# Performance work log

Measured on AMD Instinct MI355X. Metric: run time of the kernel, lower is better.

## Reference

```python
import jax, jax.numpy as jnp
import numpy as np
import math

B, T, D, CAP = 4, 1024, 512, 32768
MEM_UPDATE_MOMENTUM = 0.99
MEM_NEW_DATA_RATE = 0.01

def setup_inputs() -> dict:
    key = jax.random.key(0)
    k1, k2, k3, k4, k5 = jax.random.split(key, 5)
    keys = jax.random.normal(k1, (B, T, D), dtype=jnp.float32)
    values = jax.random.normal(k2, (B, T, D), dtype=jnp.float32)
    importance = jax.random.uniform(k3, (B, T, 1), dtype=jnp.float32)
    query = jax.random.normal(k4, (B, T, D), dtype=jnp.float32)
    # xavier_uniform on (1, CAP, D): fan_in=D, fan_out=CAP (torch treats dim-1/dim-2)
    bound = math.sqrt(6.0 / (CAP + D))
    mem = jax.random.uniform(k5, (1, CAP, D), minval=-bound, maxval=bound, dtype=jnp.float32)
    return {"keys": keys, "values": values, "importance": importance, "query": query, "mem": mem}

def reference(keys, values, importance, query, mem):
    b, t, d = keys.shape
    cap = mem.shape[1]
    # ---- write ----
    scores = jnp.einsum('btd,ocd->btc', keys, mem)          # [b, t, cap]
    usage = jax.nn.softmax(scores, axis=-1).sum(axis=1)     # [b, cap]
    combined = importance.mean(axis=(1, 2))                 # [b]
    write_priority = combined[:, None] + 0.1 * usage        # [b, cap]
    k = min(t, cap)
    _, indices = jax.lax.top_k(write_priority, k)           # [b, k]
    values_write = values[:, :k]                            # [b, k, d]
    scatter = jnp.zeros((b, cap, d), dtype=keys.dtype)
    scatter = scatter.at[jnp.arange(b)[:, None], indices].set(values_write)
    new_mem = mem * MEM_UPDATE_MOMENTUM + scatter.mean(axis=0, keepdims=True) * MEM_NEW_DATA_RATE
    # ---- read (against updated memory) ----
    attn = jnp.einsum('bqd,ocd->bqc', query, new_mem) / math.sqrt(d)
    attn = jax.nn.softmax(attn, axis=-1)                    # [b, q, cap]
    out = jnp.einsum('bqc,ocd->bqd', attn, new_mem)         # [b, q, d]
    return out
```

## Files before the change

kernel.cpp:

```cpp
#include <hip/hip_runtime.h>
#include <hip/hip_fp8.h>

typedef float f32x4 __attribute__((ext_vector_type(4)));
typedef float f32x16 __attribute__((ext_vector_type(16)));
typedef short s16x8 __attribute__((ext_vector_type(8)));
typedef short s16x4 __attribute__((ext_vector_type(4)));
typedef unsigned short ush;
typedef unsigned char u8;

constexpr int Bn = 4, Tn = 1024, Dn = 512, CAPn = 32768, Kn = 1024;
constexpr int ROWS = Bn * Tn;
constexpr float SCALE = 0.044194173824159216f;
constexpr float SC64 = SCALE / 64.0f;
constexpr float MOM = 0.99f;
constexpr float RATE_B = 0.0025f;

constexpr size_t OFF_NM8   = 0;
constexpr size_t OFF_NMT   = 33554432;
constexpr size_t OFF_OPART = 67108864;
constexpr size_t OFF_KHF   = 67108864;
constexpr size_t OFF_ZPART = 75497472;
constexpr size_t OFF_PRIO  = 83886080;
constexpr size_t OFF_RANK  = 84410368;
constexpr size_t OFF_COMB  = 84934656;
constexpr size_t OFF_ZP2   = 100663296;

#define MFMA(a, b, c) __builtin_amdgcn_mfma_f32_16x16x32_bf16((a), (b), (c), 0, 0, 0)
#define MFMAH(a, b, c) __builtin_amdgcn_mfma_f32_16x16x32_f16((a), (b), (c), 0, 0, 0)
#define MFMA8(a, b, c) __builtin_amdgcn_mfma_f32_16x16x32_fp8_fp8((a), (b), (c), 0, 0, 0)
#define MFMAB32(a, b, c) __builtin_amdgcn_mfma_f32_32x32x16_bf16((a), (b), (c), 0, 0, 0)

__device__ __forceinline__ ush bfrn(float x) {
  unsigned u = __float_as_uint(x);
  return (ush)((u + 0x7FFFu + ((u >> 16) & 1u)) >> 16);
}
__device__ __forceinline__ float bff(ush h) { return __uint_as_float(((unsigned)h) << 16); }
__device__ __forceinline__ ush f16rn(float x) {
  _Float16 h = (_Float16)x;
  return *(ush*)&h;
}
__device__ __forceinline__ u8 f8rn(float x) {
  __hip_fp8_e4m3 v(x);
  return (u8)v.__x;
}

__device__ __forceinline__ void gl16(const void* g, void* l) {
  __builtin_amdgcn_global_load_lds(
      (const __attribute__((address_space(1))) void*)(uintptr_t)g,
      (__attribute__((address_space(3))) void*)(uintptr_t)l, 16, 0, 0);
}

__global__ void k_combined(const float* __restrict__ imp, float* __restrict__ comb) {
  __shared__ float red[256];
  int b = blockIdx.x;
  float s = 0.f;
  for (int t = threadIdx.x; t < Tn; t += 256) s += imp[(size_t)b * Tn + t];
  red[threadIdx.x] = s;
  __syncthreads();
  for (int off = 128; off > 0; off >>= 1) {
    if (threadIdx.x < (unsigned)off) red[threadIdx.x] += red[threadIdx.x + off];
    __syncthreads();
  }
  if (threadIdx.x == 0) comb[b] = red[0] * (1.0f / Tn);
}

__global__ void k_cvt_f16(const float* __restrict__ x, ush* __restrict__ o) {
  size_t i = ((size_t)blockIdx.x * 256 + threadIdx.x) * 4;
  f32x4 v = *(const f32x4*)&x[i];
  s16x4 h;
#pragma unroll
  for (int j = 0; j < 4; ++j) h[j] = (short)f16rn(v[j]);
  *(s16x4*)&o[i] = h;
}

__global__ __launch_bounds__(256, 2) void k_rowexp(const ush* __restrict__ Ahf,
                                                   const ush* __restrict__ Bhf,
                                                   float* __restrict__ zpart) {
  __shared__ ush Bs[64 * 512];
  __shared__ float red[2][64];
  const int tid = threadIdx.x;
  const int lane = tid & 63, wid = tid >> 6;
  const int wc2 = wid >> 1, wt = wid & 1;
  const int l15 = lane & 15, g = lane >> 4;
  const int cb = blockIdx.x;
  const int cBase = cb * 64;

  s16x8 afr[2][16];
#pragma unroll
  for (int mi = 0; mi < 2; ++mi) {
    int c = cBase + wc2 * 32 + mi * 16 + l15;
#pragma unroll
    for (int ks = 0; ks < 16; ++ks)
      afr[mi][ks] = *(const s16x8*)&Ahf[(size_t)c * Dn + ks * 32 + g * 8];
  }

  for (int tt = 0; tt < 64; ++tt) {
    const int tBase = tt * 64;
#pragma unroll
    for (int rr = 0; rr < 16; ++rr) {
      int idx = rr * 256 + tid;
      int row = idx >> 6, ch = idx & 63;
      gl16(&Bhf[(size_t)(tBase + row) * Dn + ((ch ^ (row & 7)) << 3)],
           &Bs[rr * 2048 + wid * 512]);
    }
    __syncthreads();
    f32x4 S[2][2];
#pragma unroll
    for (int mi = 0; mi < 2; ++mi)
#pragma unroll
      for (int ni = 0; ni < 2; ++ni) S[mi][ni] = (f32x4){0.f, 0.f, 0.f, 0.f};
#pragma unroll
    for (int ks = 0; ks < 16; ++ks) {
      s16x8 bfr[2];
#pragma unroll
      for (int ni = 0; ni < 2; ++ni) {
        int trow = wt * 32 + ni * 16 + l15;
        bfr[ni] = *(const s16x8*)&Bs[trow * 512 + (((ks * 4 + g) ^ (trow & 7)) * 8)];
      }
#pragma unroll
      for (int mi = 0; mi < 2; ++mi)
#pragma unroll
        for (int ni = 0; ni < 2; ++ni) S[mi][ni] = MFMAH(afr[mi][ks], bfr[ni], S[mi][ni]);
    }
    float tacc[2] = {0.f, 0.f};
#pragma unroll
    for (int mi = 0; mi < 2; ++mi)
#pragma unroll
      for (int ni = 0; ni < 2; ++ni)
#pragma unroll
        for (int r = 0; r < 4; ++r) tacc[ni] += __expf(S[mi][ni][r]);
#pragma unroll
    for (int ni = 0; ni < 2; ++ni) {
      float v = tacc[ni];
      v += __shfl_xor(v, 16);
      v += __shfl_xor(v, 32);
      tacc[ni] = v;
    }
    if (g == 0) {
      red[wc2][wt * 32 + l15] = tacc[0];
      red[wc2][wt * 32 + 16 + l15] = tacc[1];
    }
    __syncthreads();
    if (tid < 64) zpart[(size_t)cb * ROWS + tBase + tid] = red[0][tid] + red[1][tid];
  }
}

__global__ void k_invl(const float* __restrict__ zpart, float* __restrict__ invl) {
  int t = blockIdx.x * 256 + threadIdx.x;
  float s = 0.f;
  for (int cb = 0; cb < 512; ++cb) s += zpart[(size_t)cb * ROWS + t];
  invl[t] = 1.0f / s;
}

__global__ __launch_bounds__(256, 3) void k_usage(const ush* __restrict__ mhf,
                                                  const ush* __restrict__ khf,
                                                  const float* __restrict__ invl,
                                                  const float* __restrict__ comb,
                                                  float* __restrict__ prio) {
  __shared__ ush Ah[128 * 64], Bh[128 * 64];
  const int tid = threadIdx.x;
  const int lane = tid & 63, w = tid >> 6;
  const int l15 = lane & 15, g = lane >> 4;
  const int cBase = blockIdx.x * 128;
  const int b = blockIdx.y;
  const ush* khb = khf + (size_t)b * Tn * Dn;
  const int r0 = tid >> 3, u0 = tid & 7;
  const int usw = (u0 ^ (r0 & 7)) << 3;

  float uacc[2][4] = {{0.f, 0.f, 0.f, 0.f}, {0.f, 0.f, 0.f, 0.f}};
  for (int tt = 0; tt < 8; ++tt) {
    f32x4 S[2][8];
#pragma unroll
    for (int mi = 0; mi < 2; ++mi)
#pragma unroll
      for (int ni = 0; ni < 8; ++ni) S[mi][ni] = (f32x4){0.f, 0.f, 0.f, 0.f};
    for (int kk = 0; kk < 8; ++kk) {
      __syncthreads();
      {
        size_t a0 = (size_t)(cBase + r0) * Dn + kk * 64 + usw;
        size_t a1 = (size_t)(cBase + r0 + 64) * Dn + kk * 64 + usw;
        gl16(&mhf[a0], &Ah[w * 512]);
        gl16(&mhf[a1], &Ah[4096 + w * 512]);
        size_t b0 = (size_t)(tt * 128 + r0) * Dn + kk * 64 + usw;
        size_t b1 = (size_t)(tt * 128 + r0 + 64) * Dn + kk * 64 + usw;
        gl16(&khb[b0], &Bh[w * 512]);
        gl16(&khb[b1], &Bh[4096 + w * 512]);
      }
      __syncthreads();
#pragma unroll
      for (int ks2 = 0; ks2 < 2; ++ks2) {
        s16x8 ah[2];
#pragma unroll
        for (int mi = 0; mi < 2; ++mi) {
          int crow = w * 32 + mi * 16 + l15;
          ah[mi] = *(const s16x8*)&Ah[crow * 64 + (((ks2 * 4 + g) ^ (crow & 7)) * 8)];
        }
#pragma unroll
        for (int ni = 0; ni < 8; ++ni) {
          int trow = ni * 16 + l15;
          s16x8 bh = *(const s16x8*)&Bh[trow * 64 + (((ks2 * 4 + g) ^ (trow & 7)) * 8)];
#pragma unroll
          for (int mi = 0; mi < 2; ++mi) S[mi][ni] = MFMAH(ah[mi], bh, S[mi][ni]);
        }
      }
    }
#pragma unroll
    for (int ni = 0; ni < 8; ++ni) {
      float il = invl[b * Tn + tt * 128 + ni * 16 + l15];
#pragma unroll
      for (int mi = 0; mi < 2; ++mi)
#pragma unroll
        for (int r = 0; r < 4; ++r) uacc[mi][r] += __expf(S[mi][ni][r]) * il;
    }
  }
#pragma unroll
  for (int mi = 0; mi < 2; ++mi)
#pragma unroll
    for (int r = 0; r < 4; ++r) {
      float v = uacc[mi][r];
      v += __shfl_xor(v, 1);
      v += __shfl_xor(v, 2);
      v += __shfl_xor(v, 4);
      v += __shfl_xor(v, 8);
      if (l15 == 0)
        prio[(size_t)b * CAPn + cBase + w * 32 + mi * 16 + g * 4 + r] =
            comb[b] + 0.1f * v;
    }
}

__global__ void k_rankinit(int* __restrict__ rank) {
  rank[blockIdx.x * 256 + threadIdx.x] = Kn;
}

__global__ __launch_bounds__(1024) void k_select(const float* __restrict__ prio,
                                                 int* __restrict__ rank) {
  const int b = blockIdx.x;
  const float* p = prio + (size_t)b * CAPn;
  __shared__ int hist[256];
  __shared__ unsigned long long s_pref;
  __shared__ int s_krem;
  __shared__ int s_cnt;
  __shared__ unsigned long long selk[Kn];
  const int tid = threadIdx.x;
  if (tid == 0) { s_pref = 0ull; s_krem = Kn; s_cnt = 0; }

#define KEYOF(c, kk)                                                         \
  {                                                                          \
    unsigned mb_ = __float_as_uint(p[(c)]);                                  \
    mb_ = (mb_ & 0x80000000u) ? ~mb_ : (mb_ | 0x80000000u);                  \
    (kk) = ((unsigned long long)mb_ << 32) | (unsigned)(0xFFFFFFFFu - (c));  \
  }

  __syncthreads();
  for (int pos = 56; pos >= 0; pos -= 8) {
    if (tid < 256) hist[tid] = 0;
    __syncthreads();
    unsigned long long pref = s_pref;
    unsigned long long maskhi = (pos == 56) ? 0ull : (~0ull << (pos + 8));
    for (int c = tid; c < CAPn; c += 1024) {
      unsigned long long k;
      KEYOF(c, k);
      if ((k & maskhi) == pref) atomicAdd(&hist[(int)((k >> pos) & 255)], 1);
    }
    __syncthreads();
    if (tid == 0) {
      int krem = s_krem;
      int d = 255;
      for (;; --d) {
        int h = hist[d];
        if (krem <= h || d == 0) break;
        krem -= h;
      }
      s_pref = pref | ((unsigned long long)d << pos);
      s_krem = krem;
    }
    __syncthreads();
  }
  unsigned long long T = s_pref;
  for (int c = tid; c < CAPn; c += 1024) {
    unsigned long long k;
    KEYOF(c, k);
    if (k >= T) {
      int idx = atomicAdd(&s_cnt, 1);
      selk[idx] = k;
    }
  }
  __syncthreads();
  unsigned long long mine = selk[tid];
  int r = 0;
  for (int j = 0; j < Kn; ++j) r += (selk[j] > mine) ? 1 : 0;
  int c = (int)(0xFFFFFFFFu - (unsigned)(mine & 0xFFFFFFFFull));
  rank[(size_t)b * CAPn + c] = r;
#undef KEYOF
}

__global__ void k_newmem8(const float* __restrict__ mem, const float* __restrict__ values,
                          const int* __restrict__ rank, u8* __restrict__ nm8) {
  int gid = blockIdx.x * 256 + threadIdx.x;
  int c = gid >> 7;
  int q = (gid & 127) << 2;
  f32x4 m = *(const f32x4*)&mem[(size_t)c * Dn + q];
  f32x4 acc = {0.f, 0.f, 0.f, 0.f};
#pragma unroll
  for (int b = 0; b < Bn; ++b) {
    int r = rank[(size_t)b * CAPn + c];
    if (r < Kn) acc += *(const f32x4*)&values[((size_t)b * Tn + r) * Dn + q];
  }
  f32x4 res = (m * MOM + acc * RATE_B) * 64.0f;
  union { u8 b[4]; unsigned w; } out;
#pragma unroll
  for (int j = 0; j < 4; ++j) out.b[j] = f8rn(res[j]);
  *(unsigned*)&nm8[(size_t)c * Dn + q] = out.w;
}

__global__ __launch_bounds__(256) void k_nmT(const float* __restrict__ mem,
                                             const float* __restrict__ values,
                                             const int* __restrict__ rank,
                                             ush* __restrict__ nmT) {
  __shared__ ush tile[64][65];
  int cBase = blockIdx.x * 64, dBase = blockIdx.y * 64;
  int tid = threadIdx.x;
  int c = tid >> 2, dq = (tid & 3) * 16;
  int rr[4];
#pragma unroll
  for (int b = 0; b < Bn; ++b) rr[b] = rank[(size_t)b * CAPn + cBase + c];
#pragma unroll
  for (int j = 0; j < 4; ++j) {
    f32x4 m = *(const f32x4*)&mem[(size_t)(cBase + c) * Dn + dBase + dq + j * 4];
    f32x4 a = {0.f, 0.f, 0.f, 0.f};
#pragma unroll
    for (int b = 0; b < Bn; ++b)
      if (rr[b] < Kn)
        a += *(const f32x4*)&values[((size_t)b * Tn + rr[b]) * Dn + dBase + dq + j * 4];
    f32x4 res = m * MOM + a * RATE_B;
#pragma unroll
    for (int jj = 0; jj < 4; ++jj) tile[c][dq + j * 4 + jj] = bfrn(res[jj]);
  }
  __syncthreads();
  int drow = tid >> 2, cq = (tid & 3) * 16;
#pragma unroll
  for (int k = 0; k < 2; ++k) {
    s16x8 v;
#pragma unroll
    for (int j = 0; j < 8; ++j) v[j] = (short)tile[cq + k * 8 + j][drow];
    *(s16x8*)&nmT[(size_t)(dBase + drow) * CAPn + cBase + cq + k * 8] = v;
  }
}

#define WAITV2 asm volatile("s_waitcnt vmcnt(2)" ::: "memory")
#define WAITL0 asm volatile("s_waitcnt lgkmcnt(0)" ::: "memory")
#define BAR __builtin_amdgcn_s_barrier()
__global__ __launch_bounds__(512, 1) void k_attnout(
    const float* __restrict__ query, const u8* __restrict__ nm8,
    const ush* __restrict__ nmT, ush* __restrict__ opart,
    float* __restrict__ zp2) {
  __shared__ __align__(16) u8 L[131072];
  __shared__ float zred[128];
  __shared__ float zacc[128];
  constexpr int LMS = 0, LMT = 49152, LPS = 98304;
  const int tid = threadIdx.x;
  const int lane = tid & 63, w = tid >> 6;
  const int l15 = lane & 15, g = lane >> 4;
  const int l31 = lane & 31, h = lane >> 5;
  const int dt = w & 3, qg = w >> 2;
  const int cy = blockIdx.x;
  const int qBase = blockIdx.y * 128;
  const int q = w * 16 + l15;
  const int r0 = tid >> 3, u0 = tid & 7;
  const int usw = (u0 ^ (r0 & 7)) << 3;
  const int usw8 = (u0 ^ (r0 & 7)) << 4;

  auto stage_ms = [&](int buf, int cb_, int kk) {
    const u8* src = nm8 + (size_t)cb_ * Dn + kk * 128;
    gl16(&src[(size_t)r0 * Dn + usw8], &L[LMS + buf * 16384 + w * 1024]);
    gl16(&src[(size_t)(r0 + 64) * Dn + usw8], &L[LMS + buf * 16384 + 8192 + w * 1024]);
  };
  auto stage_mt = [&](int buf, int cb_, int u) {
    const ush* src = nmT + (size_t)((u >> 1) * 128) * CAPn + cb_ + (u & 1) * 64;
    gl16(&src[(size_t)r0 * CAPn + usw], &L[LMT + buf * 16384 + w * 1024]);
    gl16(&src[(size_t)(r0 + 64) * CAPn + usw], &L[LMT + buf * 16384 + 8192 + w * 1024]);
  };

  long qfr8[16];
  {
    const float* qsrc = query + (size_t)(qBase + q) * Dn;
#pragma unroll
    for (int ks = 0; ks < 16; ++ks) {
      f32x4 a = *(const f32x4*)&qsrc[ks * 32 + g * 8];
      f32x4 b = *(const f32x4*)&qsrc[ks * 32 + g * 8 + 4];
      union { u8 c[8]; long l; } u;
#pragma unroll
      for (int j = 0; j < 4; ++j) {
        u.c[j] = f8rn(a[j]);
        u.c[4 + j] = f8rn(b[j]);
      }
      qfr8[ks] = u.l;
    }
  }

  f32x16 O[8];
#pragma unroll
  for (int i = 0; i < 8; ++i) O[i] = (f32x16)(0.f);
  if (tid < 128) zacc[tid] = 0.f;

  stage_ms(0, cy * 4096, 0);
  stage_ms(1, cy * 4096, 1);

  for (int ct = 0; ct < 32; ++ct) {
    const int cBase = cy * 4096 + ct * 128;
    const int cNext = cy * 4096 + ((ct + 1) & 31) * 128;

    f32x4 S[8];
#pragma unroll
    for (int i = 0; i < 8; ++i) S[i] = (f32x4){0.f, 0.f, 0.f, 0.f};
#pragma unroll
    for (int kk = 0; kk < 4; ++kk) {
      WAITV2;
      WAITL0;
      BAR;
      if (kk < 2) stage_ms((kk + 2) % 3, cBase, kk + 2);
      else if (kk == 2) stage_mt(0, cBase, 0);
      else stage_mt(1, cBase, 1);
      __builtin_amdgcn_s_setprio(1);
#pragma unroll
      for (int ks = 0; ks < 4; ++ks) {
#pragma unroll
        for (int mi = 0; mi < 8; ++mi) {
          int row = mi * 16 + l15;
          long a = *(const long*)&L[LMS + (kk % 3) * 16384 + row * 128 +
                                    (((ks * 2 + (g >> 1)) ^ (row & 7)) << 4) +
                                    (g & 1) * 8];
          S[mi] = MFMA8(a, qfr8[kk * 4 + ks], S[mi]);
        }
      }
      __builtin_amdgcn_s_setprio(0);
    }

    float zl = 0.f;
#pragma unroll
    for (int mi = 0; mi < 8; ++mi) {
      s16x4 p;
#pragma unroll
      for (int r = 0; r < 4; ++r) {
        float e = __expf(S[mi][r] * SC64);
        zl += e;
        p[r] = (short)bfrn(e);
      }
      int u16 = (mi * 2 + (g >> 1)) ^ l15;
      *(s16x4*)&L[LPS + q * 256 + u16 * 16 + (g & 1) * 8] = p;
    }
    zl += __shfl_xor(zl, 16);
    zl += __shfl_xor(zl, 32);
    if (g == 0) zred[q] = zl;
    WAITL0;
    BAR;
    if (tid < 128) zacc[tid] += zred[tid];

#pragma unroll
    for (int u = 0; u < 8; ++u) {
      WAITV2;
      WAITL0;
      BAR;
      if (u < 6) stage_mt((u + 2) % 3, cBase, u + 2);
      else if (u == 6) stage_ms(0, cNext, 0);
      else stage_ms(1, cNext, 1);
      __builtin_amdgcn_s_setprio(1);
#pragma unroll
      for (int kc = 0; kc < 4; ++kc) {
        int d = dt * 32 + l31;
        s16x8 am = *(const s16x8*)&L[LMT + (u % 3) * 16384 + d * 128 +
                                     (((kc * 2 + h) ^ (d & 7)) << 4)];
#pragma unroll
        for (int tqi = 0; tqi < 2; ++tqi) {
          int qq = qg * 64 + tqi * 32 + l31;
          s16x8 pb = *(const s16x8*)&L[LPS + qq * 256 +
                                       ((((u & 1) * 8 + kc * 2 + h) ^ (qq & 15)) << 4)];
          O[(u >> 1) * 2 + tqi] = MFMAB32(am, pb, O[(u >> 1) * 2 + tqi]);
        }
      }
      __builtin_amdgcn_s_setprio(0);
    }
  }

  __syncthreads();
  if (tid < 128) zp2[(size_t)cy * ROWS + qBase + tid] = zacc[tid];
#pragma unroll
  for (int p = 0; p < 4; ++p) {
    __syncthreads();
    if (qg == (p >> 1)) {
      const int tqi = p & 1;
#pragma unroll
      for (int db = 0; db < 4; ++db)
#pragma unroll
        for (int r2 = 0; r2 < 4; ++r2) {
          s16x4 ov;
#pragma unroll
          for (int j = 0; j < 4; ++j) ov[j] = (short)bfrn(O[db * 2 + tqi][r2 * 4 + j]);
          int u8i = db * 32 + dt * 8 + r2 * 2 + h;
          int u8s = u8i ^ ((l31 & 15) << 1);
          *(s16x4*)&L[LPS + l31 * 1024 + u8s * 8] = ov;
        }
    }
    __syncthreads();
#pragma unroll
    for (int i = 0; i < 4; ++i) {
      int slot = i * 512 + tid;
      int ql = slot >> 6, u16 = slot & 63;
      s16x8 v = *(const s16x8*)&L[LPS + ql * 1024 + ((u16 ^ (ql & 15)) << 4)];
      *(s16x8*)&opart[((size_t)cy * ROWS + qBase + p * 32 + ql) * Dn + u16 * 8] = v;
    }
  }
}

__global__ void k_merge(const ush* __restrict__ opart, const float* __restrict__ zp2,
                        float* __restrict__ out) {
  size_t i = ((size_t)blockIdx.x * 256 + threadIdx.x) * 4;
  int row = (int)(i >> 9);
  float z = 0.f;
#pragma unroll
  for (int cyy = 0; cyy < 8; ++cyy) z += zp2[(size_t)cyy * ROWS + row];
  float inv = 1.0f / z;
  f32x4 acc = {0.f, 0.f, 0.f, 0.f};
#pragma unroll
  for (int cyy = 0; cyy < 8; ++cyy) {
    s16x4 a = *(const s16x4*)&opart[(size_t)cyy * ROWS * Dn + i];
#pragma unroll
    for (int j = 0; j < 4; ++j) acc[j] += bff((ush)a[j]);
  }
#pragma unroll
  for (int j = 0; j < 4; ++j) acc[j] *= inv;
  *(f32x4*)&out[i] = acc;
}

extern "C" void kernel_launch(void* const* d_in, const int* in_sizes, int n_in,
                              void* d_out, int out_size, void* d_ws, size_t ws_size,
                              hipStream_t stream) {
  const float* keys = (const float*)d_in[0];
  const float* values = (const float*)d_in[1];
  const float* importance = (const float*)d_in[2];
  const float* query = (const float*)d_in[3];
  const float* mem = (const float*)d_in[4];
  char* wsb = (char*)d_ws;
  u8* nm8    = (u8*)(wsb + OFF_NM8);
  ush* nmT   = (ush*)(wsb + OFF_NMT);
  ush* mhf   = (ush*)(wsb + OFF_NMT);
  ush* khf   = (ush*)(wsb + OFF_KHF);
  ush* opart = (ush*)(wsb + OFF_OPART);
  float* zpart = (float*)(wsb + OFF_ZPART);
  float* prio  = (float*)(wsb + OFF_PRIO);
  int* rank    = (int*)(wsb + OFF_RANK);
  float* comb  = (float*)(wsb + OFF_COMB);
  float* zp2   = (float*)(wsb + OFF_ZP2);
  float* invl1 = (float*)(wsb + OFF_COMB + 64);
  float* out = (float*)d_out;

  k_combined<<<Bn, 256, 0, stream>>>(importance, comb);
  k_cvt_f16<<<(ROWS * Dn / 4) / 256, 256, 0, stream>>>(keys, khf);
  k_cvt_f16<<<(CAPn * Dn / 4) / 256, 256, 0, stream>>>(mem, mhf);
  k_rowexp<<<CAPn / 64, 256, 0, stream>>>(mhf, khf, zpart);
  k_invl<<<ROWS / 256, 256, 0, stream>>>(zpart, invl1);
  k_usage<<<dim3(CAPn / 128, Bn), 256, 0, stream>>>(mhf, khf, invl1, comb, prio);
  k_rankinit<<<(Bn * CAPn) / 256, 256, 0, stream>>>(rank);
  k_select<<<Bn, 1024, 0, stream>>>(prio, rank);
  k_newmem8<<<(CAPn * Dn / 4) / 256, 256, 0, stream>>>(mem, values, rank, nm8);
  k_nmT<<<dim3(CAPn / 64, Dn / 64), 256, 0, stream>>>(mem, values, rank, nmT);
  k_attnout<<<dim3(8, ROWS / 128), 512, 0, stream>>>(query, nm8, nmT, opart, zp2);
  k_merge<<<(ROWS * Dn / 4) / 256, 256, 0, stream>>>(opart, zp2, out);
}
```

Measured before the change: 855.4 us.

## Keep mem fragments in registers and double-buffer key tiles in k_usage

k_usage now loads its mem (A) fragments once into registers for the whole D dimension, so mem tiles are no longer re-staged through LDS on every step. Key tiles are double-buffered in LDS, with the next tile prefetched after a single barrier, and the MFMA block runs under raised wave priority. The two f16 conversion launches are also merged into one kernel. In exchange, register pressure rises (occupancy hint drops from 3 to 2) and the prefetch waits on vmcnt(0), which limits how much load latency can overlap with compute.

```diff
diff --git a/kernel.cpp b/kernel.cpp
--- a/kernel.cpp
+++ b/kernel.cpp
@@ -64,13 +64,26 @@
   if (threadIdx.x == 0) comb[b] = red[0] * (1.0f / Tn);
 }
 
-__global__ void k_cvt_f16(const float* __restrict__ x, ush* __restrict__ o) {
-  size_t i = ((size_t)blockIdx.x * 256 + threadIdx.x) * 4;
-  f32x4 v = *(const f32x4*)&x[i];
+__global__ void k_cvt_all(const float* __restrict__ mem, const float* __restrict__ keys,
+                          ush* __restrict__ mhf, ush* __restrict__ khf) {
+  int bid = blockIdx.x;
+  const float* src;
+  ush* dst;
+  size_t i;
+  if (bid < 16384) {
+    src = mem;
+    dst = mhf;
+    i = ((size_t)bid * 256 + threadIdx.x) * 4;
+  } else {
+    src = keys;
+    dst = khf;
+    i = ((size_t)(bid - 16384) * 256 + threadIdx.x) * 4;
+  }
+  f32x4 v = *(const f32x4*)&src[i];
   s16x4 h;
 #pragma unroll
   for (int j = 0; j < 4; ++j) h[j] = (short)f16rn(v[j]);
-  *(s16x4*)&o[i] = h;
+  *(s16x4*)&dst[i] = h;
 }
 
 __global__ __launch_bounds__(256, 2) void k_rowexp(const ush* __restrict__ Ahf,
@@ -152,12 +165,17 @@
   invl[t] = 1.0f / s;
 }
 
-__global__ __launch_bounds__(256, 3) void k_usage(const ush* __restrict__ mhf,
+#define WAITV0 asm volatile("s_waitcnt vmcnt(0)" ::: "memory")
+#define WAITV2 asm volatile("s_waitcnt vmcnt(2)" ::: "memory")
+#define WAITL0 asm volatile("s_waitcnt lgkmcnt(0)" ::: "memory")
+#define BAR __builtin_amdgcn_s_barrier()
+
+__global__ __launch_bounds__(256, 2) void k_usage(const ush* __restrict__ mhf,
                                                   const ush* __restrict__ khf,
                                                   const float* __restrict__ invl,
                                                   const float* __restrict__ comb,
                                                   float* __restrict__ prio) {
-  __shared__ ush Ah[128 * 64], Bh[128 * 64];
+  __shared__ ush Bh[2][128 * 64];
   const int tid = threadIdx.x;
   const int lane = tid & 63, w = tid >> 6;
   const int l15 = lane & 15, g = lane >> 4;
@@ -167,42 +185,52 @@
   const int r0 = tid >> 3, u0 = tid & 7;
   const int usw = (u0 ^ (r0 & 7)) << 3;
 
+  s16x8 afr[2][16];
+#pragma unroll
+  for (int mi = 0; mi < 2; ++mi) {
+    int c = cBase + w * 32 + mi * 16 + l15;
+#pragma unroll
+    for (int ks = 0; ks < 16; ++ks)
+      afr[mi][ks] = *(const s16x8*)&mhf[(size_t)c * Dn + ks * 32 + g * 8];
+  }
+
+  auto stageB = [&](int p) {
+    int tt = p >> 3, kk = p & 7;
+    size_t b0 = (size_t)(tt * 128 + r0) * Dn + kk * 64 + usw;
+    size_t b1 = (size_t)(tt * 128 + r0 + 64) * Dn + kk * 64 + usw;
+    gl16(&khb[b0], &Bh[p & 1][w * 512]);
+    gl16(&khb[b1], &Bh[p & 1][4096 + w * 512]);
+  };
+
   float uacc[2][4] = {{0.f, 0.f, 0.f, 0.f}, {0.f, 0.f, 0.f, 0.f}};
+  stageB(0);
   for (int tt = 0; tt < 8; ++tt) {
     f32x4 S[2][8];
 #pragma unroll
     for (int mi = 0; mi < 2; ++mi)
 #pragma unroll
       for (int ni = 0; ni < 8; ++ni) S[mi][ni] = (f32x4){0.f, 0.f, 0.f, 0.f};
+#pragma unroll
     for (int kk = 0; kk < 8; ++kk) {
-      __syncthreads();
-      {
-        size_t a0 = (size_t)(cBase + r0) * Dn + kk * 64 + usw;
-        size_t a1 = (size_t)(cBase + r0 + 64) * Dn + kk * 64 + usw;
-        gl16(&mhf[a0], &Ah[w * 512]);
-        gl16(&mhf[a1], &Ah[4096 + w * 512]);
-        size_t b0 = (size_t)(tt * 128 + r0) * Dn + kk * 64 + usw;
-        size_t b1 = (size_t)(tt * 128 + r0 + 64) * Dn + kk * 64 + usw;
-        gl16(&khb[b0], &Bh[w * 512]);
-        gl16(&khb[b1], &Bh[4096 + w * 512]);
-      }
-      __syncthreads();
+      const int p = tt * 8 + kk;
+      WAITV0;
+      WAITL0;
+      BAR;
+      if (p < 63) stageB(p + 1);
+      __builtin_amdgcn_s_setprio(1);
 #pragma unroll
       for (int ks2 = 0; ks2 < 2; ++ks2) {
-        s16x8 ah[2];
-#pragma unroll
-        for (int mi = 0; mi < 2; ++mi) {
-          int crow = w * 32 + mi * 16 + l15;
-          ah[mi] = *(const s16x8*)&Ah[crow * 64 + (((ks2 * 4 + g) ^ (crow & 7)) * 8)];
-        }
 #pragma unroll
         for (int ni = 0; ni < 8; ++ni) {
           int trow = ni * 16 + l15;
-          s16x8 bh = *(const s16x8*)&Bh[trow * 64 + (((ks2 * 4 + g) ^ (trow & 7)) * 8)];
-#pragma unroll
-          for (int mi = 0; mi < 2; ++mi) S[mi][ni] = MFMAH(ah[mi], bh, S[mi][ni]);
+          s16x8 bh =
+              *(const s16x8*)&Bh[p & 1][trow * 64 + (((ks2 * 4 + g) ^ (trow & 7)) * 8)];
+#pragma unroll
+          for (int mi = 0; mi < 2; ++mi)
+            S[mi][ni] = MFMAH(afr[mi][kk * 2 + ks2], bh, S[mi][ni]);
         }
       }
+      __builtin_amdgcn_s_setprio(0);
     }
 #pragma unroll
     for (int ni = 0; ni < 8; ++ni) {
@@ -347,9 +375,6 @@
   }
 }
 
-#define WAITV2 asm volatile("s_waitcnt vmcnt(2)" ::: "memory")
-#define WAITL0 asm volatile("s_waitcnt lgkmcnt(0)" ::: "memory")
-#define BAR __builtin_amdgcn_s_barrier()
 __global__ __launch_bounds__(512, 1) void k_attnout(
     const float* __restrict__ query, const u8* __restrict__ nm8,
     const ush* __restrict__ nmT, ush* __restrict__ opart,
@@ -555,8 +580,7 @@
   float* out = (float*)d_out;
 
   k_combined<<<Bn, 256, 0, stream>>>(importance, comb);
-  k_cvt_f16<<<(ROWS * Dn / 4) / 256, 256, 0, stream>>>(keys, khf);
-  k_cvt_f16<<<(CAPn * Dn / 4) / 256, 256, 0, stream>>>(mem, mhf);
+  k_cvt_all<<<18432, 256, 0, stream>>>(mem, keys, mhf, khf);
   k_rowexp<<<CAPn / 64, 256, 0, stream>>>(mhf, khf, zpart);
   k_invl<<<ROWS / 256, 256, 0, stream>>>(zpart, invl1);
   k_usage<<<dim3(CAPn / 128, Bn), 256, 0, stream>>>(mhf, khf, invl1, comb, prio);
```

Result: faster. 789.1 us (-7.7%).
